# Performance work log

Hardware: AMD Instinct MI355X
Metric: run time of the kernel (lower is better)

Reference implementation:

```python
import jax, jax.numpy as jnp
import numpy as np

MAX_OBJECTS = 20
NODE_FEAT_DIM = 16
N_COLORS = 10
N_OPS = 8
HID = 64
RANK = 4
B = 32768


def _layer_norm(x, gamma, beta, eps=1e-5):
    mu = x.mean(-1, keepdims=True)
    var = ((x - mu) ** 2).mean(-1, keepdims=True)
    return (x - mu) / jnp.sqrt(var + eps) * gamma + beta


def setup_inputs() -> dict:
    key = jax.random.key(0)
    ks = jax.random.split(key, 32)
    lin = lambda k, i, o: jax.random.normal(k, (i, o), jnp.float32) * (1.0 / np.sqrt(i))
    d = {}
    d['nf'] = jax.random.normal(ks[0], (B, MAX_OBJECTS, NODE_FEAT_DIM), jnp.float32)
    d['nn_c'] = jax.random.randint(ks[1], (B,), 1, MAX_OBJECTS + 1)
    # ne + its LoRA adapter
    d['ne_W'] = lin(ks[2], NODE_FEAT_DIM, HID); d['ne_b'] = jnp.zeros((HID,), jnp.float32)
    d['ne_A'] = jax.random.normal(ks[3], (NODE_FEAT_DIM, RANK), jnp.float32) * 0.01
    d['ne_B'] = jax.random.normal(ks[4], (RANK, HID), jnp.float32) * 0.01
    # g1: Linear(2*hid,hid) [LoRA-wrapped] then Linear(hid,hid); relu applied after in lora path
    d['g1_W0'] = lin(ks[5], 2 * HID, HID); d['g1_b0'] = jnp.zeros((HID,), jnp.float32)
    d['g1_A'] = jax.random.normal(ks[6], (2 * HID, RANK), jnp.float32) * 0.01
    d['g1_B'] = jax.random.normal(ks[7], (RANK, HID), jnp.float32) * 0.01
    d['g1_W2'] = lin(ks[8], HID, HID); d['g1_b2'] = jnp.zeros((HID,), jnp.float32)
    d['g2_W0'] = lin(ks[9], 2 * HID, HID); d['g2_b0'] = jnp.zeros((HID,), jnp.float32)
    d['g2_A'] = jax.random.normal(ks[10], (2 * HID, RANK), jnp.float32) * 0.01
    d['g2_B'] = jax.random.normal(ks[11], (RANK, HID), jnp.float32) * 0.01
    d['g2_W2'] = lin(ks[12], HID, HID); d['g2_b2'] = jnp.zeros((HID,), jnp.float32)
    d['n1_g'] = jnp.ones((HID,), jnp.float32); d['n1_b'] = jnp.zeros((HID,), jnp.float32)
    d['n2_g'] = jnp.ones((HID,), jnp.float32); d['n2_b'] = jnp.zeros((HID,), jnp.float32)
    d['oh_W'] = lin(ks[13], HID, N_OPS); d['oh_b'] = jnp.zeros((N_OPS,), jnp.float32)
    d['c1_W'] = lin(ks[14], HID, N_COLORS); d['c1_b'] = jnp.zeros((N_COLORS,), jnp.float32)
    d['c2_W'] = lin(ks[15], HID, N_COLORS); d['c2_b'] = jnp.zeros((N_COLORS,), jnp.float32)
    d['pq_W'] = lin(ks[16], HID, HID); d['pq_b'] = jnp.zeros((HID,), jnp.float32)
    d['pk_W'] = lin(ks[17], HID, HID); d['pk_b'] = jnp.zeros((HID,), jnp.float32)
    return d


def reference(nf, nn_c, ne_W, ne_b, ne_A, ne_B,
              g1_W0, g1_b0, g1_A, g1_B, g1_W2, g1_b2,
              g2_W0, g2_b0, g2_A, g2_B, g2_W2, g2_b2,
              n1_g, n1_b, n2_g, n2_b,
              oh_W, oh_b, c1_W, c1_b, c2_W, c2_b, pq_W, pq_b, pk_W, pk_b):
    mask = jnp.arange(MAX_OBJECTS)[None, :] < nn_c[:, None]            # [B, N]
    mf = mask.astype(nf.dtype)[..., None]                              # [B, N, 1]
    denom = jnp.clip(mf.sum(1, keepdims=True), 1.0, None)              # [B, 1, 1]

    # node embedding with LoRA
    h = nf @ ne_W + ne_b + (nf @ ne_A) @ ne_B                          # [B, N, hid]

    def gnn_layer(h, W0, b0, A, Bm, W2, b2, lg, lb):
        msg = (h * mf).sum(1, keepdims=True) / denom                   # [B, 1, hid]
        cat = jnp.concatenate([h, jnp.broadcast_to(msg, h.shape)], -1) # [B, N, 2*hid]
        z = cat @ W0 + b0 + (cat @ A) @ Bm                             # LoRA linear
        h = h + jax.nn.relu(z @ W2 + b2)                               # relu AFTER second linear (lora path)
        return _layer_norm(h, lg, lb) * mf

    h = gnn_layer(h, g1_W0, g1_b0, g1_A, g1_B, g1_W2, g1_b2, n1_g, n1_b)
    h = gnn_layer(h, g2_W0, g2_b0, g2_A, g2_B, g2_W2, g2_b2, n2_g, n2_b)

    g = (h * mf).sum(1) / jnp.clip(mf.sum(1), 1.0, None)               # [B, hid]
    q = g @ pq_W + pq_b                                                # [B, hid]
    k = h @ pk_W + pk_b                                                # [B, N, hid]
    pl = jnp.einsum('bd,bnd->bn', q, k)
    pl = jnp.where(mask, pl, jnp.float32(-1e9))
    return (g @ oh_W + oh_b, g @ c1_W + c1_b, g @ c2_W + c2_b, pl, g)
```

## Files before the change

kernel.cpp:

```cpp
#include <hip/hip_runtime.h>

static constexpr int BATCH = 32768;

typedef short bf8 __attribute__((ext_vector_type(8)));
typedef float f32x4 __attribute__((ext_vector_type(4)));
typedef unsigned short u16x4 __attribute__((ext_vector_type(4)));

#define MFMA16 __builtin_amdgcn_mfma_f32_16x16x32_bf16


__device__ __forceinline__ unsigned short f2bf(float f) {
    return __builtin_bit_cast(unsigned short, static_cast<__bf16>(f));
}
__device__ __forceinline__ float bf2f(unsigned short h) {
    return __uint_as_float(((unsigned)h) << 16);
}

#define SWI(row, col)  ((row) * 64 + ((col) ^ (((row) & 7) << 3)))
#define LD8(buf, row, col8) (*(const bf8*)((buf) + (row) * 64 + 8 * ((col8) ^ ((row) & 7))))

__global__ void __launch_bounds__(256) merge_all(
    const float* __restrict__ neW, const float* __restrict__ neA, const float* __restrict__ neB,
    const float* __restrict__ ne_b,
    const float* __restrict__ g1W0, const float* __restrict__ g1A, const float* __restrict__ g1B,
    const float* __restrict__ g1W2, const float* __restrict__ g1b0, const float* __restrict__ g1b2,
    const float* __restrict__ g2W0, const float* __restrict__ g2A, const float* __restrict__ g2B,
    const float* __restrict__ g2W2, const float* __restrict__ g2b0, const float* __restrict__ g2b2,
    const float* __restrict__ pkW, const float* __restrict__ pqW,
    const float* __restrict__ ohW, const float* __restrict__ c1W, const float* __restrict__ c2W,
    const float* __restrict__ ohb, const float* __restrict__ c1b, const float* __restrict__ c2b,
    unsigned short* __restrict__ ws) {
    int t = blockIdx.x * 256 + threadIdx.x;
    if (t >= 28832) return;
    if (t >= 28768) {
        int n = t - 28768;
        float acc = g2b2[n];
        for (int k = 0; k < 64; ++k) acc = fmaf(g2b0[k], g2W2[k * 64 + n], acc);
        ((float*)ws)[14432 + n] = acc;
        return;
    }
    if (t >= 28704) {
        int n = t - 28704;
        float acc = g1b2[n];
        for (int k = 0; k < 64; ++k) acc = fmaf(g1b0[k], g1W2[k * 64 + n], acc);
        ((float*)ws)[14368 + n] = acc;
        return;
    }
    if (t >= 28672) {
        int i = t - 28672;
        float v = 0.0f;
        if (i < 8) v = ohb[i]; else if (i < 18) v = c1b[i - 8]; else if (i < 28) v = c2b[i - 18];
        ((float*)ws)[14336 + i] = v;
        return;
    }
    float val = 0.0f;
    if (t < 2048) {
        int n = t >> 5, k = t & 31;
        if (k < 16) {
            val = neW[k * 64 + n];
            #pragma unroll
            for (int r = 0; r < 4; ++r) val = fmaf(neA[k * 4 + r], neB[r * 64 + n], val);
        } else if (k == 16) {
            val = ne_b[n];
        }
    } else if (t < 18432) {
        int loc = t - 2048;
        const float *W0, *A, *Bm, *W2;
        if (loc < 8192) { W0 = g1W0; A = g1A; Bm = g1B; W2 = g1W2; }
        else { loc -= 8192; W0 = g2W0; A = g2A; Bm = g2B; W2 = g2W2; }
        int n = loc >> 7, k = loc & 127;
        float a0 = A[k * 4 + 0], a1 = A[k * 4 + 1], a2 = A[k * 4 + 2], a3 = A[k * 4 + 3];
        for (int j = 0; j < 64; ++j) {
            float w0e = W0[k * 64 + j];
            w0e = fmaf(a0, Bm[0 * 64 + j], w0e);
            w0e = fmaf(a1, Bm[1 * 64 + j], w0e);
            w0e = fmaf(a2, Bm[2 * 64 + j], w0e);
            w0e = fmaf(a3, Bm[3 * 64 + j], w0e);
            val = fmaf(w0e, W2[j * 64 + n], val);
        }
    } else if (t < 22528) {
        int loc = t - 18432; int n = loc >> 6, k = loc & 63;
        val = pkW[k * 64 + n];
    } else if (t < 26624) {
        int loc = t - 22528; int n = loc >> 6, k = loc & 63;
        val = pqW[k * 64 + n];
    } else {
        int loc = t - 26624; int n = loc >> 6, k = loc & 63;
        if (n < 8) val = ohW[k * 8 + n];
        else if (n < 18) val = c1W[k * 10 + (n - 8)];
        else if (n < 28) val = c2W[k * 10 + (n - 18)];
    }
    ws[t] = f2bf(val);
}

__device__ __forceinline__ int nc_sel(int4 nc, int bb) {
    int lo = (bb & 1) ? nc.y : nc.x;
    int hi = (bb & 1) ? nc.w : nc.z;
    return (bb & 2) ? hi : lo;
}

__device__ __forceinline__ void wave_mean(
    const unsigned short* hbuf, unsigned short* msgbuf, float* out4,
    int4 nc, int b0, int g, int c) {
    int c4 = c * 4;
    float s0 = 0, s1 = 0, s2 = 0, s3 = 0;
    int base = g * 20;
    #pragma unroll
    for (int n = 0; n < 20; ++n) {
        int row = base + n;
        u16x4 v = *(const u16x4*)(hbuf + SWI(row, c4));
        s0 += bf2f(v[0]); s1 += bf2f(v[1]); s2 += bf2f(v[2]); s3 += bf2f(v[3]);
    }
    float ic = 1.0f / (float)nc_sel(nc, g);
    s0 *= ic; s1 *= ic; s2 *= ic; s3 *= ic;
    u16x4 o; o[0] = f2bf(s0); o[1] = f2bf(s1); o[2] = f2bf(s2); o[3] = f2bf(s3);
    *(u16x4*)(msgbuf + SWI(g, c4)) = o;
    if (out4) {
        f32x4 fo = {s0, s1, s2, s3};
        *(f32x4*)(out4 + (size_t)(b0 + g) * 64 + c4) = fo;
    }
}

__device__ __forceinline__ void gnn_layer_sw(
    unsigned short* hbuf, unsigned short* msgbuf,
    const unsigned short* __restrict__ w02t,
    const float* __restrict__ b2e, const float* __restrict__ gmp, const float* __restrict__ btp,
    int4 nc, unsigned vmask, int b0, int g, int c) {
    wave_mean(hbuf, msgbuf, nullptr, nc, b0, g, c);
    const int nb = g * 4;

    #pragma unroll 1
    for (int mt = 0; mt < 5; ++mt) {
        int rA = mt * 16 + c;
        int bA = (rA >= 20) + (rA >= 40) + (rA >= 60);
        bf8 h0 = LD8(hbuf, rA, 0 + g);
        bf8 h1 = LD8(hbuf, rA, 4 + g);
        bf8 m0 = LD8(msgbuf, bA, 0 + g);
        bf8 m1 = LD8(msgbuf, bA, 4 + g);
        f32x4 du[4];
        #pragma unroll
        for (int nt = 0; nt < 4; ++nt) du[nt] = (f32x4){0.f, 0.f, 0.f, 0.f};
        #pragma unroll
        for (int nt = 0; nt < 4; ++nt) {
            const unsigned short* wp = w02t + (nt * 16 + c) * 128 + g * 8;
            du[nt] = MFMA16(*(const bf8*)(wp), h0, du[nt], 0, 0, 0);
            du[nt] = MFMA16(*(const bf8*)(wp + 32), h1, du[nt], 0, 0, 0);
            du[nt] = MFMA16(*(const bf8*)(wp + 64), m0, du[nt], 0, 0, 0);
            du[nt] = MFMA16(*(const bf8*)(wp + 96), m1, du[nt], 0, 0, 0);
        }
        float vv[16];
        float ps = 0.f, pq = 0.f;
        #pragma unroll
        for (int nt = 0; nt < 4; ++nt) {
            f32x4 b4 = *(const f32x4*)(b2e + nt * 16 + nb);
            u16x4 h4 = *(const u16x4*)(hbuf + SWI(rA, nt * 16 + nb));
            #pragma unroll
            for (int r = 0; r < 4; ++r) {
                float u = du[nt][r] + b4[r];
                float v = bf2f(h4[r]) + fmaxf(u, 0.f);
                vv[nt * 4 + r] = v;
                ps += v; pq += v * v;
            }
        }
        ps += __shfl_xor(ps, 16, 64); ps += __shfl_xor(ps, 32, 64);
        pq += __shfl_xor(pq, 16, 64); pq += __shfl_xor(pq, 32, 64);
        float mu = ps * 0.015625f;
        float var = pq * 0.015625f - mu * mu;
        float rstd = rsqrtf(var + 1e-5f);
        bool valid = (vmask >> mt) & 1u;
        #pragma unroll
        for (int nt = 0; nt < 4; ++nt) {
            f32x4 g4 = *(const f32x4*)(gmp + nt * 16 + nb);
            f32x4 t4 = *(const f32x4*)(btp + nt * 16 + nb);
            u16x4 o;
            #pragma unroll
            for (int r = 0; r < 4; ++r) {
                float hn = (vv[nt * 4 + r] - mu) * rstd * g4[r] + t4[r];
                o[r] = f2bf(valid ? hn : 0.f);
            }
            *(u16x4*)(hbuf + SWI(rA, nt * 16 + nb)) = o;
        }
    }
}

__global__ void __launch_bounds__(64) gnn_main(
    const float* __restrict__ nf, const int* __restrict__ nn_c,
    const unsigned short* __restrict__ W,
    const float* __restrict__ n1g, const float* __restrict__ n1b,
    const float* __restrict__ n2g, const float* __restrict__ n2b,
    const float* __restrict__ pqb, const float* __restrict__ pkb,
    float* __restrict__ out) {
    __shared__ __align__(16) unsigned short hbuf[80 * 64];
    __shared__ __align__(16) unsigned short msgbuf[4 * 64];
    __shared__ __align__(16) float qbuf[4 * 68];

    const int lane = threadIdx.x & 63;
    const int g = lane >> 4, c = lane & 15;
    const int nb = g * 4;
    const int b0 = blockIdx.x * 4;
    const long grow0 = (long)b0 * 20;

    const unsigned short* neWt  = W;
    const unsigned short* w02t1 = W + 2048;
    const unsigned short* w02t2 = W + 10240;
    const unsigned short* pkt   = W + 18432;
    const unsigned short* pqt   = W + 22528;
    const unsigned short* hdt   = W + 26624;
    const float* wsf = (const float*)W;
    const float* headb = wsf + 14336;

    const size_t OUT1 = (size_t)BATCH * 8,  OUT2 = (size_t)BATCH * 18;
    const size_t OUT3 = (size_t)BATCH * 28, OUT4 = (size_t)BATCH * 48;

    int4 nc;
    nc.x = nn_c[b0 + 0]; nc.y = nn_c[b0 + 1];
    nc.z = nn_c[b0 + 2]; nc.w = nn_c[b0 + 3];

    unsigned vmask = 0;

    {
        bf8 bne[4];
        #pragma unroll
        for (int nt = 0; nt < 4; ++nt)
            bne[nt] = *(const bf8*)(neWt + (nt * 16 + c) * 32 + g * 8);
        #pragma unroll 1
        for (int mt = 0; mt < 5; ++mt) {
            int rA = mt * 16 + c;
            int bq = (rA >= 20) + (rA >= 40) + (rA >= 60);
            bf8 b = (bf8){0, 0, 0, 0, 0, 0, 0, 0};
            if (g < 2) {
                const f32x4* p4 = (const f32x4*)(nf + (grow0 + rA) * 16 + g * 8);
                f32x4 x = p4[0], y = p4[1];
                b[0] = (short)f2bf(x[0]); b[1] = (short)f2bf(x[1]);
                b[2] = (short)f2bf(x[2]); b[3] = (short)f2bf(x[3]);
                b[4] = (short)f2bf(y[0]); b[5] = (short)f2bf(y[1]);
                b[6] = (short)f2bf(y[2]); b[7] = (short)f2bf(y[3]);
            } else if (g == 2) {
                b[0] = (short)0x3F80;
            }
            f32x4 acc[4];
            #pragma unroll
            for (int nt = 0; nt < 4; ++nt) acc[nt] = (f32x4){0.f, 0.f, 0.f, 0.f};
            #pragma unroll
            for (int nt = 0; nt < 4; ++nt) acc[nt] = MFMA16(bne[nt], b, acc[nt], 0, 0, 0);
            bool valid = (rA - bq * 20) < nc_sel(nc, bq);
            vmask |= (valid ? 1u : 0u) << mt;
            #pragma unroll
            for (int nt = 0; nt < 4; ++nt) {
                u16x4 o;
                #pragma unroll
                for (int r = 0; r < 4; ++r) o[r] = f2bf(valid ? acc[nt][r] : 0.f);
                *(u16x4*)(hbuf + SWI(rA, nt * 16 + nb)) = o;
            }
        }
    }

    gnn_layer_sw(hbuf, msgbuf, w02t1, wsf + 14368, n1g, n1b, nc, vmask, b0, g, c);
    gnn_layer_sw(hbuf, msgbuf, w02t2, wsf + 14432, n2g, n2b, nc, vmask, b0, g, c);

    wave_mean(hbuf, msgbuf, out + OUT4, nc, b0, g, c);

    {
        bf8 a0 = LD8(msgbuf, (c & 3), 0 + g);
        bf8 a1 = LD8(msgbuf, (c & 3), 4 + g);
        f32x4 dq[4];
        #pragma unroll
        for (int nt = 0; nt < 4; ++nt) dq[nt] = (f32x4){0.f, 0.f, 0.f, 0.f};
        #pragma unroll
        for (int nt = 0; nt < 4; ++nt) {
            const unsigned short* wp = pqt + (nt * 16 + c) * 64 + g * 8;
            dq[nt] = MFMA16(a0, *(const bf8*)(wp), dq[nt], 0, 0, 0);
            dq[nt] = MFMA16(a1, *(const bf8*)(wp + 32), dq[nt], 0, 0, 0);
        }
        f32x4 dh[2];
        #pragma unroll
        for (int nt = 0; nt < 2; ++nt) dh[nt] = (f32x4){0.f, 0.f, 0.f, 0.f};
        #pragma unroll
        for (int nt = 0; nt < 2; ++nt) {
            const unsigned short* wp = hdt + (nt * 16 + c) * 64 + g * 8;
            dh[nt] = MFMA16(a0, *(const bf8*)(wp), dh[nt], 0, 0, 0);
            dh[nt] = MFMA16(a1, *(const bf8*)(wp + 32), dh[nt], 0, 0, 0);
        }
        if (g == 0) {
            #pragma unroll
            for (int r = 0; r < 4; ++r) {
                #pragma unroll
                for (int nt = 0; nt < 4; ++nt)
                    qbuf[r * 68 + nt * 16 + c] = dq[nt][r] + pqb[nt * 16 + c];
                size_t ob = (size_t)(b0 + r);
                #pragma unroll
                for (int nt = 0; nt < 2; ++nt) {
                    int col = nt * 16 + c;
                    float v = dh[nt][r] + headb[col];
                    if (col < 8)       out[ob * 8 + col] = v;
                    else if (col < 18) out[OUT1 + ob * 10 + (col - 8)] = v;
                    else if (col < 28) out[OUT2 + ob * 10 + (col - 18)] = v;
                }
            }
        }
    }

    {
        #pragma unroll 1
        for (int mt = 0; mt < 5; ++mt) {
            int rA = mt * 16 + c;
            int bA = (rA >= 20) + (rA >= 40) + (rA >= 60);
            bf8 h0 = LD8(hbuf, rA, 0 + g);
            bf8 h1 = LD8(hbuf, rA, 4 + g);
            f32x4 dk[4];
            #pragma unroll
            for (int nt = 0; nt < 4; ++nt) dk[nt] = (f32x4){0.f, 0.f, 0.f, 0.f};
            #pragma unroll
            for (int nt = 0; nt < 4; ++nt) {
                const unsigned short* wp = pkt + (nt * 16 + c) * 64 + g * 8;
                dk[nt] = MFMA16(*(const bf8*)(wp), h0, dk[nt], 0, 0, 0);
                dk[nt] = MFMA16(*(const bf8*)(wp + 32), h1, dk[nt], 0, 0, 0);
            }
            float pl = 0.f;
            #pragma unroll
            for (int nt = 0; nt < 4; ++nt) {
                f32x4 q4 = *(const f32x4*)(&qbuf[bA * 68 + nt * 16 + nb]);
                f32x4 p4 = *(const f32x4*)(pkb + nt * 16 + nb);
                #pragma unroll
                for (int r = 0; r < 4; ++r)
                    pl = fmaf(dk[nt][r] + p4[r], q4[r], pl);
            }
            pl += __shfl_xor(pl, 16, 64);
            pl += __shfl_xor(pl, 32, 64);
            if (g == 0) {
                bool valid = (vmask >> mt) & 1u;
                out[OUT3 + (size_t)(grow0 + rA)] = valid ? pl : -1e9f;
            }
        }
    }
}

extern "C" void kernel_launch(void* const* d_in, const int* in_sizes, int n_in,
                              void* d_out, int out_size, void* d_ws, size_t ws_size,
                              hipStream_t stream) {
    const float* nf   = (const float*)d_in[0];
    const int*   nn_c = (const int*)d_in[1];
    const float* neW  = (const float*)d_in[2];
    const float* ne_b = (const float*)d_in[3];
    const float* neA  = (const float*)d_in[4];
    const float* neB  = (const float*)d_in[5];
    const float* g1W0 = (const float*)d_in[6];
    const float* g1b0 = (const float*)d_in[7];
    const float* g1A  = (const float*)d_in[8];
    const float* g1B  = (const float*)d_in[9];
    const float* g1W2 = (const float*)d_in[10];
    const float* g1b2 = (const float*)d_in[11];
    const float* g2W0 = (const float*)d_in[12];
    const float* g2b0 = (const float*)d_in[13];
    const float* g2A  = (const float*)d_in[14];
    const float* g2B  = (const float*)d_in[15];
    const float* g2W2 = (const float*)d_in[16];
    const float* g2b2 = (const float*)d_in[17];
    const float* n1g  = (const float*)d_in[18];
    const float* n1b  = (const float*)d_in[19];
    const float* n2g  = (const float*)d_in[20];
    const float* n2b  = (const float*)d_in[21];
    const float* ohW  = (const float*)d_in[22];
    const float* ohb  = (const float*)d_in[23];
    const float* c1W  = (const float*)d_in[24];
    const float* c1b  = (const float*)d_in[25];
    const float* c2W  = (const float*)d_in[26];
    const float* c2b  = (const float*)d_in[27];
    const float* pqW  = (const float*)d_in[28];
    const float* pqb  = (const float*)d_in[29];
    const float* pkW  = (const float*)d_in[30];
    const float* pkb  = (const float*)d_in[31];
    unsigned short* ws = (unsigned short*)d_ws;
    float* out = (float*)d_out;

    merge_all<<<113, 256, 0, stream>>>(neW, neA, neB, ne_b,
                                       g1W0, g1A, g1B, g1W2, g1b0, g1b2,
                                       g2W0, g2A, g2B, g2W2, g2b0, g2b2,
                                       pkW, pqW, ohW, c1W, c2W,
                                       ohb, c1b, c2b, ws);
    gnn_main<<<BATCH / 4, 64, 0, stream>>>(nf, nn_c, ws,
                                           n1g, n1b, n2g, n2b,
                                           pqb, pkb, out);
}
```

Baseline: 104.3 us.

## Reassociate pointer logits as h·(Wk q) and prefetch next GNN row tiles

The pointer-logit stage no longer computes k = h@Wk for every node. It first forms w = Wk·q per batch element (plus the scalar q·bk) with a small MFMA on a bf16 copy of q, then takes a dot product of each node's h with w. This drops most of the MFMA work in that stage, but q is now rounded to bf16 and the summation order changes. Separately, the GNN layer loop loads the next tile's h and msg fragments before the epilogue, so LDS reads overlap with the normalization math.

```diff
diff --git a/kernel.cpp b/kernel.cpp
--- a/kernel.cpp
+++ b/kernel.cpp
@@ -79,8 +79,7 @@
             val = fmaf(w0e, W2[j * 64 + n], val);
         }
     } else if (t < 22528) {
-        int loc = t - 18432; int n = loc >> 6, k = loc & 63;
-        val = pkW[k * 64 + n];
+        val = pkW[t - 18432];
     } else if (t < 26624) {
         int loc = t - 22528; int n = loc >> 6, k = loc & 63;
         val = pqW[k * 64 + n];
@@ -129,14 +128,14 @@
     wave_mean(hbuf, msgbuf, nullptr, nc, b0, g, c);
     const int nb = g * 4;
 
+    bf8 h0 = LD8(hbuf, c, 0 + g);
+    bf8 h1 = LD8(hbuf, c, 4 + g);
+    bf8 m0 = LD8(msgbuf, 0, 0 + g);
+    bf8 m1 = LD8(msgbuf, 0, 4 + g);
+
     #pragma unroll 1
     for (int mt = 0; mt < 5; ++mt) {
         int rA = mt * 16 + c;
-        int bA = (rA >= 20) + (rA >= 40) + (rA >= 60);
-        bf8 h0 = LD8(hbuf, rA, 0 + g);
-        bf8 h1 = LD8(hbuf, rA, 4 + g);
-        bf8 m0 = LD8(msgbuf, bA, 0 + g);
-        bf8 m1 = LD8(msgbuf, bA, 4 + g);
         f32x4 du[4];
         #pragma unroll
         for (int nt = 0; nt < 4; ++nt) du[nt] = (f32x4){0.f, 0.f, 0.f, 0.f};
@@ -147,6 +146,14 @@
             du[nt] = MFMA16(*(const bf8*)(wp + 32), h1, du[nt], 0, 0, 0);
             du[nt] = MFMA16(*(const bf8*)(wp + 64), m0, du[nt], 0, 0, 0);
             du[nt] = MFMA16(*(const bf8*)(wp + 96), m1, du[nt], 0, 0, 0);
+        }
+        if (mt < 4) {
+            int rN = rA + 16;
+            int bN = (rN >= 20) + (rN >= 40) + (rN >= 60);
+            h0 = LD8(hbuf, rN, 0 + g);
+            h1 = LD8(hbuf, rN, 4 + g);
+            m0 = LD8(msgbuf, bN, 0 + g);
+            m1 = LD8(msgbuf, bN, 4 + g);
         }
         float vv[16];
         float ps = 0.f, pq = 0.f;
@@ -192,7 +199,8 @@
     float* __restrict__ out) {
     __shared__ __align__(16) unsigned short hbuf[80 * 64];
     __shared__ __align__(16) unsigned short msgbuf[4 * 64];
-    __shared__ __align__(16) float qbuf[4 * 68];
+    __shared__ __align__(16) unsigned short qbufh[4 * 64];
+    __shared__ __align__(16) float wbuf[4 * 72];
 
     const int lane = threadIdx.x & 63;
     const int g = lane >> 4, c = lane & 15;
@@ -203,7 +211,7 @@
     const unsigned short* neWt  = W;
     const unsigned short* w02t1 = W + 2048;
     const unsigned short* w02t2 = W + 10240;
-    const unsigned short* pkt   = W + 18432;
+    const unsigned short* pkwt  = W + 18432;
     const unsigned short* pqt   = W + 22528;
     const unsigned short* hdt   = W + 26624;
     const float* wsf = (const float*)W;
@@ -286,7 +294,7 @@
             for (int r = 0; r < 4; ++r) {
                 #pragma unroll
                 for (int nt = 0; nt < 4; ++nt)
-                    qbuf[r * 68 + nt * 16 + c] = dq[nt][r] + pqb[nt * 16 + c];
+                    qbufh[r * 64 + nt * 16 + c] = f2bf(dq[nt][r] + pqb[nt * 16 + c]);
                 size_t ob = (size_t)(b0 + r);
                 #pragma unroll
                 for (int nt = 0; nt < 2; ++nt) {
@@ -301,29 +309,43 @@
     }
 
     {
+        bf8 qb0 = *(const bf8*)(qbufh + (c & 3) * 64 + g * 8);
+        bf8 qb1 = *(const bf8*)(qbufh + (c & 3) * 64 + 32 + g * 8);
+        #pragma unroll
+        for (int jt = 0; jt < 4; ++jt) {
+            const unsigned short* wp = pkwt + (jt * 16 + c) * 64 + g * 8;
+            f32x4 dw = (f32x4){0.f, 0.f, 0.f, 0.f};
+            dw = MFMA16(*(const bf8*)(wp), qb0, dw, 0, 0, 0);
+            dw = MFMA16(*(const bf8*)(wp + 32), qb1, dw, 0, 0, 0);
+            if (c < 4)
+                *(f32x4*)(wbuf + c * 72 + jt * 16 + g * 4) = dw;
+        }
+        u16x4 q4 = *(const u16x4*)(qbufh + g * 64 + c * 4);
+        f32x4 p4 = *(const f32x4*)(pkb + c * 4);
+        float plc = bf2f(q4[0]) * p4[0];
+        plc = fmaf(bf2f(q4[1]), p4[1], plc);
+        plc = fmaf(bf2f(q4[2]), p4[2], plc);
+        plc = fmaf(bf2f(q4[3]), p4[3], plc);
+        plc += __shfl_xor(plc, 1, 64);
+        plc += __shfl_xor(plc, 2, 64);
+        plc += __shfl_xor(plc, 4, 64);
+        plc += __shfl_xor(plc, 8, 64);
+        if (c == 0) wbuf[g * 72 + 64] = plc;
+    }
+
+    {
         #pragma unroll 1
         for (int mt = 0; mt < 5; ++mt) {
             int rA = mt * 16 + c;
             int bA = (rA >= 20) + (rA >= 40) + (rA >= 60);
-            bf8 h0 = LD8(hbuf, rA, 0 + g);
-            bf8 h1 = LD8(hbuf, rA, 4 + g);
-            f32x4 dk[4];
-            #pragma unroll
-            for (int nt = 0; nt < 4; ++nt) dk[nt] = (f32x4){0.f, 0.f, 0.f, 0.f};
+            float pl = wbuf[bA * 72 + 64];
             #pragma unroll
             for (int nt = 0; nt < 4; ++nt) {
-                const unsigned short* wp = pkt + (nt * 16 + c) * 64 + g * 8;
-                dk[nt] = MFMA16(*(const bf8*)(wp), h0, dk[nt], 0, 0, 0);
-                dk[nt] = MFMA16(*(const bf8*)(wp + 32), h1, dk[nt], 0, 0, 0);
-            }
-            float pl = 0.f;
-            #pragma unroll
-            for (int nt = 0; nt < 4; ++nt) {
-                f32x4 q4 = *(const f32x4*)(&qbuf[bA * 68 + nt * 16 + nb]);
-                f32x4 p4 = *(const f32x4*)(pkb + nt * 16 + nb);
+                u16x4 h4 = *(const u16x4*)(hbuf + SWI(rA, nt * 16 + nb));
+                f32x4 w4 = *(const f32x4*)(wbuf + bA * 72 + nt * 16 + nb);
                 #pragma unroll
                 for (int r = 0; r < 4; ++r)
-                    pl = fmaf(dk[nt][r] + p4[r], q4[r], pl);
+                    pl = fmaf(bf2f(h4[r]), w4[r], pl);
             }
             pl += __shfl_xor(pl, 16, 64);
             pl += __shfl_xor(pl, 32, 64);
```

After: 108.5 us. 4.0% more time.
